# Performance work log

Hardware: AMD Instinct MI355X
Metric: run time of the kernel (lower is better)

## Reference

```python
import jax, jax.numpy as jnp
import numpy as np

N_IN, N_HID, N_OUT = 128, 128, 128
BATCH = 131072

def _linear_params(key, fan_in, fan_out):
    # torch nn.Linear default init: U(-1/sqrt(fan_in), 1/sqrt(fan_in))
    kw, kb = jax.random.split(key)
    bound = 1.0 / np.sqrt(fan_in)
    W = jax.random.uniform(kw, (fan_out, fan_in), jnp.float32, -bound, bound)
    b = jax.random.uniform(kb, (fan_out,), jnp.float32, -bound, bound)
    return W, b

def setup_inputs() -> dict:
    key = jax.random.key(0)
    ks = jax.random.split(key, 6)
    x = jax.random.normal(ks[0], (BATCH, N_IN), jnp.float32)
    hidden = jnp.zeros((BATCH, N_HID), jnp.float32)
    ctx = jnp.zeros((BATCH, N_HID), jnp.float32)
    Wf, bf = _linear_params(ks[1], N_IN + N_HID, N_HID)
    Wi, bi = _linear_params(ks[2], N_IN + N_HID, N_HID)
    Wc, bc = _linear_params(ks[3], N_IN + N_HID, N_HID)
    Wo, bo = _linear_params(ks[4], N_IN + N_HID, N_HID)
    Wfc, bfc = _linear_params(ks[5], N_HID, N_OUT)
    return {"x": x, "hidden": hidden, "ctx": ctx,
            "Wf": Wf, "bf": bf, "Wi": Wi, "bi": bi,
            "Wc": Wc, "bc": bc, "Wo": Wo, "bo": bo,
            "Wfc": Wfc, "bfc": bfc}

def reference(x, hidden, ctx, Wf, bf, Wi, bi, Wc, bc, Wo, bo, Wfc, bfc):
    # cat order matches torch: (hidden, x)
    cat_input = jnp.concatenate([hidden, x], axis=1)  # [B, n_hid+n_in]
    # Stack the four gate weights into one GEMM, then split (same math).
    W4 = jnp.concatenate([Wf, Wi, Wc, Wo], axis=0)    # [4*n_hid, n_hid+n_in]
    b4 = jnp.concatenate([bf, bi, bc, bo], axis=0)
    gates = cat_input @ W4.T + b4                     # [B, 4*n_hid]
    f_lin, i_lin, c_lin, o_lin = jnp.split(gates, 4, axis=1)
    f_t = jax.nn.sigmoid(f_lin)
    i_t = jax.nn.sigmoid(i_lin)
    c_t_temp = jnp.tanh(c_lin)
    ctx_new = f_t * ctx + i_t * c_t_temp
    o_t = jax.nn.sigmoid(o_lin)
    hidden_new = o_t * jnp.tanh(ctx_new)
    out = hidden_new @ Wfc.T + bfc                    # [B, n_out]
    return (out, hidden_new, ctx_new)
```

## Files before the change

### kernel.cpp

```cpp
#include <hip/hip_runtime.h>

#define BATCH   131072
#define NHID    128
#define KDIM    256
#define BM      32
#define TPB     512
#define NBLK    256
#define NTILE   (BATCH / BM)
#define TPBLK   (NTILE / NBLK)

typedef __bf16 bf16_t;
typedef __bf16 bf16x4 __attribute__((ext_vector_type(4)));
typedef __bf16 bf16x8 __attribute__((ext_vector_type(8)));
typedef float  f32x4  __attribute__((ext_vector_type(4)));

__device__ __forceinline__ float fsigmoid(float v) {
    return __builtin_amdgcn_rcpf(1.0f + __builtin_amdgcn_exp2f(v * -1.44269504f));
}
__device__ __forceinline__ float ftanh(float v) {
    return __builtin_fmaf(-2.0f,
        __builtin_amdgcn_rcpf(1.0f + __builtin_amdgcn_exp2f(v * 2.88539008f)), 1.0f);
}
__device__ __forceinline__ f32x4 vsig(f32x4 v) {
    f32x4 r;
    #pragma unroll
    for (int i = 0; i < 4; ++i) r[i] = fsigmoid(v[i]);
    return r;
}
__device__ __forceinline__ f32x4 vtanh(f32x4 v) {
    f32x4 r;
    #pragma unroll
    for (int i = 0; i < 4; ++i) r[i] = ftanh(v[i]);
    return r;
}

__global__ void prep_kernel(const float* __restrict__ Wf, const float* __restrict__ Wi,
                            const float* __restrict__ Wc, const float* __restrict__ Wo,
                            const float* __restrict__ bfp, const float* __restrict__ bip,
                            const float* __restrict__ bcp, const float* __restrict__ bop,
                            const float* __restrict__ Wfc,
                            bf16_t* __restrict__ W4p, float* __restrict__ b4p,
                            bf16_t* __restrict__ Wfcb)
{
    int id = blockIdx.x * 256 + threadIdx.x;
    if (id < 512 * 256) {
        int p = id >> 8, k = id & 255;
        int w = p >> 6, t = (p >> 4) & 3, c = p & 15;
        int j = w * 16 + c;
        const float* W = (t == 0) ? Wf : (t == 1) ? Wi : (t == 2) ? Wc : Wo;
        W4p[id] = (bf16_t)W[j * 256 + k];
        if (k == 0) {
            const float* bs = (t == 0) ? bfp : (t == 1) ? bip : (t == 2) ? bcp : bop;
            b4p[p] = bs[j];
        }
    } else {
        int id2 = id - 512 * 256;
        if (id2 < 128 * 128) Wfcb[id2] = (bf16_t)Wfc[id2];
    }
}

__global__ __launch_bounds__(TPB, 2) void lstm_fused(
    const float* __restrict__ x, const float* __restrict__ hidden, const float* __restrict__ ctx,
    const bf16_t* __restrict__ W4p, const float* __restrict__ b4p,
    const bf16_t* __restrict__ Wfcb, const float* __restrict__ bfc,
    float* __restrict__ out, float* __restrict__ hid_out, float* __restrict__ ctx_out)
{
    __shared__ __align__(16) char lds[2 * 16384 + 2 * 8192];

    const int tid  = threadIdx.x;
    const int lane = tid & 63;
    const int wv   = tid >> 6;
    const int l16  = lane & 15;
    const int lq   = lane >> 4;
    const int tile0 = blockIdx.x * TPBLK;
    const int colb  = wv * 16 + lq * 4;
    const int swzA  = (l16 & 7) << 4;

    const int r_s = tid >> 4;
    const int c_s = tid & 15;
    const int swzS = (r_s & 7) << 4;

    bf16x8 B1[32];
    {
        const bf16_t* Bp = W4p + (wv * 64 + l16) * 256 + lq * 8;
        #pragma unroll
        for (int pm = 0; pm < 4; ++pm)
            #pragma unroll
            for (int ks = 0; ks < 8; ++ks)
                B1[pm * 8 + ks] = *(const bf16x8*)(Bp + pm * 16 * 256 + ks * 32);
    }
    bf16x8 b2r[4];
    {
        const bf16_t* B2 = Wfcb + (wv * 16 + l16) * 128 + lq * 8;
        #pragma unroll
        for (int ks = 0; ks < 4; ++ks) b2r[ks] = *(const bf16x8*)(B2 + ks * 32);
    }
    const f32x4 bf4 = *(const f32x4*)(b4p + wv * 64 +  0 + lq * 4);
    const f32x4 bi4 = *(const f32x4*)(b4p + wv * 64 + 16 + lq * 4);
    const f32x4 bc4 = *(const f32x4*)(b4p + wv * 64 + 32 + lq * 4);
    const f32x4 bo4 = *(const f32x4*)(b4p + wv * 64 + 48 + lq * 4);
    const f32x4 bfc4 = *(const f32x4*)(bfc + colb);

    f32x4 sv0, sv1, sv2, sv3;
    f32x4 ctxA[2], ctxB[2];

    {
        const int grow = tile0 * BM + r_s;
        const float* hrow = hidden + (size_t)grow * NHID + c_s * 4;
        const float* xrow = x      + (size_t)grow * NHID + c_s * 4;
        f32x4 t0 = *(const f32x4*)(hrow);
        f32x4 t1 = *(const f32x4*)(hrow + 64);
        f32x4 t2 = *(const f32x4*)(xrow);
        f32x4 t3 = *(const f32x4*)(xrow + 64);
        char* A0 = lds;
        bf16x4 p0, p1, p2, p3;
        p0[0]=(bf16_t)t0.x; p0[1]=(bf16_t)t0.y; p0[2]=(bf16_t)t0.z; p0[3]=(bf16_t)t0.w;
        p1[0]=(bf16_t)t1.x; p1[1]=(bf16_t)t1.y; p1[2]=(bf16_t)t1.z; p1[3]=(bf16_t)t1.w;
        p2[0]=(bf16_t)t2.x; p2[1]=(bf16_t)t2.y; p2[2]=(bf16_t)t2.z; p2[3]=(bf16_t)t2.w;
        p3[0]=(bf16_t)t3.x; p3[1]=(bf16_t)t3.y; p3[2]=(bf16_t)t3.z; p3[3]=(bf16_t)t3.w;
        *(bf16x4*)(A0 + r_s * 512 + ((c_s * 8 +   0) ^ swzS)) = p0;
        *(bf16x4*)(A0 + r_s * 512 + ((c_s * 8 + 128) ^ swzS)) = p1;
        *(bf16x4*)(A0 + r_s * 512 + ((c_s * 8 + 256) ^ swzS)) = p2;
        *(bf16x4*)(A0 + r_s * 512 + ((c_s * 8 + 384) ^ swzS)) = p3;
    }
    {
        const float* cp = ctx + (size_t)(tile0 * BM) * NHID + colb;
        ctxA[0] = *(const f32x4*)(cp + (size_t)l16 * NHID);
        ctxA[1] = *(const f32x4*)(cp + (size_t)(16 + l16) * NHID);
    }
    __syncthreads();

    for (int t = 0; t < TPBLK; ++t) {
        const int P = t & 1;
        const int row0 = (tile0 + t) * BM;
        char* Asb = lds + P * 16384;
        char* Hsb = lds + 32768 + P * 8192;

        {
            const int tn = (t + 1 < TPBLK) ? t + 1 : TPBLK - 1;
            const int grow = (tile0 + tn) * BM + r_s;
            const float* hrow = hidden + (size_t)grow * NHID + c_s * 4;
            const float* xrow = x      + (size_t)grow * NHID + c_s * 4;
            sv0 = *(const f32x4*)(hrow);
            sv1 = *(const f32x4*)(hrow + 64);
            sv2 = *(const f32x4*)(xrow);
            sv3 = *(const f32x4*)(xrow + 64);
            const float* cp = ctx + (size_t)((tile0 + tn) * BM) * NHID + colb;
            ctxB[0] = *(const f32x4*)(cp + (size_t)l16 * NHID);
            ctxB[1] = *(const f32x4*)(cp + (size_t)(16 + l16) * NHID);
        }

        f32x4 acc[4][2];
        #pragma unroll
        for (int pm = 0; pm < 4; ++pm) {
            acc[pm][0] = f32x4{0.f, 0.f, 0.f, 0.f};
            acc[pm][1] = f32x4{0.f, 0.f, 0.f, 0.f};
        }
        #pragma unroll
        for (int ks = 0; ks < 8; ++ks) {
            const int kb = ks * 64 + lq * 16;
            bf16x8 a0 = *(const bf16x8*)(Asb + l16 * 512        + (kb ^ swzA));
            bf16x8 a1 = *(const bf16x8*)(Asb + (16 + l16) * 512 + (kb ^ swzA));
            #pragma unroll
            for (int pm = 0; pm < 4; ++pm) {
                acc[pm][0] = __builtin_amdgcn_mfma_f32_16x16x32_bf16(B1[pm * 8 + ks], a0, acc[pm][0], 0, 0, 0);
                acc[pm][1] = __builtin_amdgcn_mfma_f32_16x16x32_bf16(B1[pm * 8 + ks], a1, acc[pm][1], 0, 0, 0);
            }
        }

        #pragma unroll
        for (int bn = 0; bn < 2; ++bn) {
            const size_t grow = (size_t)(row0 + bn * 16 + l16) * NHID + colb;
            const f32x4 fv = vsig(acc[0][bn] + bf4);
            const f32x4 iv = vsig(acc[1][bn] + bi4);
            const f32x4 cv = vtanh(acc[2][bn] + bc4);
            const f32x4 ov = vsig(acc[3][bn] + bo4);
            const f32x4 cn = fv * ctxA[bn] + iv * cv;
            const f32x4 hn = ov * vtanh(cn);
            *(f32x4*)(ctx_out + grow) = cn;
            *(f32x4*)(hid_out + grow) = hn;
            bf16x4 hb;
            hb[0] = (bf16_t)hn.x; hb[1] = (bf16_t)hn.y;
            hb[2] = (bf16_t)hn.z; hb[3] = (bf16_t)hn.w;
            const int rh = bn * 16 + l16;
            *(bf16x4*)(Hsb + rh * 256 + ((wv * 32 + lq * 8) ^ ((rh & 7) << 4))) = hb;
        }
        ctxA[0] = ctxB[0];
        ctxA[1] = ctxB[1];

        {
            char* An = lds + (1 - P) * 16384;
            bf16x4 p0, p1, p2, p3;
            p0[0]=(bf16_t)sv0.x; p0[1]=(bf16_t)sv0.y; p0[2]=(bf16_t)sv0.z; p0[3]=(bf16_t)sv0.w;
            p1[0]=(bf16_t)sv1.x; p1[1]=(bf16_t)sv1.y; p1[2]=(bf16_t)sv1.z; p1[3]=(bf16_t)sv1.w;
            p2[0]=(bf16_t)sv2.x; p2[1]=(bf16_t)sv2.y; p2[2]=(bf16_t)sv2.z; p2[3]=(bf16_t)sv2.w;
            p3[0]=(bf16_t)sv3.x; p3[1]=(bf16_t)sv3.y; p3[2]=(bf16_t)sv3.z; p3[3]=(bf16_t)sv3.w;
            *(bf16x4*)(An + r_s * 512 + ((c_s * 8 +   0) ^ swzS)) = p0;
            *(bf16x4*)(An + r_s * 512 + ((c_s * 8 + 128) ^ swzS)) = p1;
            *(bf16x4*)(An + r_s * 512 + ((c_s * 8 + 256) ^ swzS)) = p2;
            *(bf16x4*)(An + r_s * 512 + ((c_s * 8 + 384) ^ swzS)) = p3;
        }

        __syncthreads();

        f32x4 acc2[2];
        acc2[0] = f32x4{0.f, 0.f, 0.f, 0.f};
        acc2[1] = f32x4{0.f, 0.f, 0.f, 0.f};
        #pragma unroll
        for (int ks = 0; ks < 4; ++ks) {
            const int kb = ks * 64 + lq * 16;
            bf16x8 h0 = *(const bf16x8*)(Hsb + l16 * 256        + (kb ^ swzA));
            bf16x8 h1 = *(const bf16x8*)(Hsb + (16 + l16) * 256 + (kb ^ swzA));
            acc2[0] = __builtin_amdgcn_mfma_f32_16x16x32_bf16(b2r[ks], h0, acc2[0], 0, 0, 0);
            acc2[1] = __builtin_amdgcn_mfma_f32_16x16x32_bf16(b2r[ks], h1, acc2[1], 0, 0, 0);
        }
        #pragma unroll
        for (int bn = 0; bn < 2; ++bn) {
            const size_t grow = (size_t)(row0 + bn * 16 + l16) * NHID + colb;
            *(f32x4*)(out + grow) = acc2[bn] + bfc4;
        }
    }
}

extern "C" void kernel_launch(void* const* d_in, const int* in_sizes, int n_in,
                              void* d_out, int out_size, void* d_ws, size_t ws_size,
                              hipStream_t stream) {
    const float* x      = (const float*)d_in[0];
    const float* hidden = (const float*)d_in[1];
    const float* ctx    = (const float*)d_in[2];
    const float* Wf     = (const float*)d_in[3];
    const float* bfp    = (const float*)d_in[4];
    const float* Wi     = (const float*)d_in[5];
    const float* bip    = (const float*)d_in[6];
    const float* Wc     = (const float*)d_in[7];
    const float* bcp    = (const float*)d_in[8];
    const float* Wo     = (const float*)d_in[9];
    const float* bop    = (const float*)d_in[10];
    const float* Wfc    = (const float*)d_in[11];
    const float* bfc    = (const float*)d_in[12];

    bf16_t* W4p  = (bf16_t*)d_ws;
    float*  b4p  = (float*)((char*)d_ws + 512 * 256 * 2);
    bf16_t* Wfcb = (bf16_t*)((char*)d_ws + 512 * 256 * 2 + 2048);

    prep_kernel<<<576, 256, 0, stream>>>(Wf, Wi, Wc, Wo, bfp, bip, bcp, bop, Wfc,
                                         W4p, b4p, Wfcb);

    float* outp = (float*)d_out;
    lstm_fused<<<NBLK, TPB, 0, stream>>>(
        x, hidden, ctx, W4p, b4p, Wfcb, bfc,
        outp,
        outp + (size_t)BATCH * NHID,
        outp + 2 * (size_t)BATCH * NHID);
}
```

Baseline: 117.0 us.

## Stage fp32 input tiles directly into LDS via global_load_lds

Replaces the register-staged load, bf16 convert and LDS store of the hidden/x tile with asynchronous global_load_lds transfers of raw fp32 data into a swizzled LDS buffer. The bf16 conversion moves into the MFMA operand read path. The ctx/hidden output stores are also moved after the barrier. The aim is to free VGPRs and VALU work from staging and overlap loads better, at the cost of doubling LDS footprint (dynamic shared memory) and LDS read traffic, plus extra conversions inside the inner GEMM loop.

```diff
diff --git a/kernel.cpp b/kernel.cpp
--- a/kernel.cpp
+++ b/kernel.cpp
@@ -9,10 +9,17 @@
 #define NTILE   (BATCH / BM)
 #define TPBLK   (NTILE / NBLK)
 
+#define AS_BYTES  (BM * KDIM * 4)
+#define HS_BYTES  (BM * NHID * 2)
+#define LDS_TOTAL (2 * AS_BYTES + 2 * HS_BYTES)
+
 typedef __bf16 bf16_t;
 typedef __bf16 bf16x4 __attribute__((ext_vector_type(4)));
 typedef __bf16 bf16x8 __attribute__((ext_vector_type(8)));
 typedef float  f32x4  __attribute__((ext_vector_type(4)));
+
+#define LDS_AS3(p)  ((__attribute__((address_space(3))) void*)(p))
+#define GLB_AS1(p)  ((const __attribute__((address_space(1))) void*)(p))
 
 __device__ __forceinline__ float fsigmoid(float v) {
     return __builtin_amdgcn_rcpf(1.0f + __builtin_amdgcn_exp2f(v * -1.44269504f));
@@ -65,7 +72,7 @@
     const bf16_t* __restrict__ Wfcb, const float* __restrict__ bfc,
     float* __restrict__ out, float* __restrict__ hid_out, float* __restrict__ ctx_out)
 {
-    __shared__ __align__(16) char lds[2 * 16384 + 2 * 8192];
+    extern __shared__ __align__(16) char smem[];
 
     const int tid  = threadIdx.x;
     const int lane = tid & 63;
@@ -74,11 +81,6 @@
     const int lq   = lane >> 4;
     const int tile0 = blockIdx.x * TPBLK;
     const int colb  = wv * 16 + lq * 4;
-    const int swzA  = (l16 & 7) << 4;
-
-    const int r_s = tid >> 4;
-    const int c_s = tid & 15;
-    const int swzS = (r_s & 7) << 4;
 
     bf16x8 B1[32];
     {
@@ -95,34 +97,29 @@
         #pragma unroll
         for (int ks = 0; ks < 4; ++ks) b2r[ks] = *(const bf16x8*)(B2 + ks * 32);
     }
-    const f32x4 bf4 = *(const f32x4*)(b4p + wv * 64 +  0 + lq * 4);
-    const f32x4 bi4 = *(const f32x4*)(b4p + wv * 64 + 16 + lq * 4);
-    const f32x4 bc4 = *(const f32x4*)(b4p + wv * 64 + 32 + lq * 4);
-    const f32x4 bo4 = *(const f32x4*)(b4p + wv * 64 + 48 + lq * 4);
+    const f32x4 bf4  = *(const f32x4*)(b4p + wv * 64 +  0 + lq * 4);
+    const f32x4 bi4  = *(const f32x4*)(b4p + wv * 64 + 16 + lq * 4);
+    const f32x4 bc4  = *(const f32x4*)(b4p + wv * 64 + 32 + lq * 4);
+    const f32x4 bo4  = *(const f32x4*)(b4p + wv * 64 + 48 + lq * 4);
     const f32x4 bfc4 = *(const f32x4*)(bfc + colb);
 
-    f32x4 sv0, sv1, sv2, sv3;
     f32x4 ctxA[2], ctxB[2];
 
-    {
-        const int grow = tile0 * BM + r_s;
-        const float* hrow = hidden + (size_t)grow * NHID + c_s * 4;
-        const float* xrow = x      + (size_t)grow * NHID + c_s * 4;
-        f32x4 t0 = *(const f32x4*)(hrow);
-        f32x4 t1 = *(const f32x4*)(hrow + 64);
-        f32x4 t2 = *(const f32x4*)(xrow);
-        f32x4 t3 = *(const f32x4*)(xrow + 64);
-        char* A0 = lds;
-        bf16x4 p0, p1, p2, p3;
-        p0[0]=(bf16_t)t0.x; p0[1]=(bf16_t)t0.y; p0[2]=(bf16_t)t0.z; p0[3]=(bf16_t)t0.w;
-        p1[0]=(bf16_t)t1.x; p1[1]=(bf16_t)t1.y; p1[2]=(bf16_t)t1.z; p1[3]=(bf16_t)t1.w;
-        p2[0]=(bf16_t)t2.x; p2[1]=(bf16_t)t2.y; p2[2]=(bf16_t)t2.z; p2[3]=(bf16_t)t2.w;
-        p3[0]=(bf16_t)t3.x; p3[1]=(bf16_t)t3.y; p3[2]=(bf16_t)t3.z; p3[3]=(bf16_t)t3.w;
-        *(bf16x4*)(A0 + r_s * 512 + ((c_s * 8 +   0) ^ swzS)) = p0;
-        *(bf16x4*)(A0 + r_s * 512 + ((c_s * 8 + 128) ^ swzS)) = p1;
-        *(bf16x4*)(A0 + r_s * 512 + ((c_s * 8 + 256) ^ swzS)) = p2;
-        *(bf16x4*)(A0 + r_s * 512 + ((c_s * 8 + 384) ^ swzS)) = p3;
-    }
+    #define STAGE_TILE(An, tt) do {                                             \
+        const int rowb = (tt) * BM;                                             \
+        _Pragma("unroll")                                                       \
+        for (int i = 0; i < 4; ++i) {                                           \
+            const int r = wv * 4 + i;                                           \
+            const int qs = (lane * 16) ^ ((r & 15) << 4);                       \
+            const char* sp = (qs < 512)                                         \
+                ? ((const char*)hidden + (size_t)(rowb + r) * 512 + qs)         \
+                : ((const char*)x      + (size_t)(rowb + r) * 512 + (qs - 512));\
+            __builtin_amdgcn_global_load_lds(GLB_AS1(sp),                       \
+                LDS_AS3((An) + r * 1024), 16, 0, 0);                            \
+        }                                                                       \
+    } while (0)
+
+    STAGE_TILE(smem, tile0 - tile0 + tile0 * 0 + tile0);
     {
         const float* cp = ctx + (size_t)(tile0 * BM) * NHID + colb;
         ctxA[0] = *(const f32x4*)(cp + (size_t)l16 * NHID);
@@ -133,19 +130,14 @@
     for (int t = 0; t < TPBLK; ++t) {
         const int P = t & 1;
         const int row0 = (tile0 + t) * BM;
-        char* Asb = lds + P * 16384;
-        char* Hsb = lds + 32768 + P * 8192;
+        char* Asb = smem + P * AS_BYTES;
+        char* Hsb = smem + 2 * AS_BYTES + P * HS_BYTES;
 
         {
-            const int tn = (t + 1 < TPBLK) ? t + 1 : TPBLK - 1;
-            const int grow = (tile0 + tn) * BM + r_s;
-            const float* hrow = hidden + (size_t)grow * NHID + c_s * 4;
-            const float* xrow = x      + (size_t)grow * NHID + c_s * 4;
-            sv0 = *(const f32x4*)(hrow);
-            sv1 = *(const f32x4*)(hrow + 64);
-            sv2 = *(const f32x4*)(xrow);
-            sv3 = *(const f32x4*)(xrow + 64);
-            const float* cp = ctx + (size_t)((tile0 + tn) * BM) * NHID + colb;
+            const int tn = (t + 1 < TPBLK) ? (tile0 + t + 1) : (tile0 + TPBLK - 1);
+            char* An = smem + (1 - P) * AS_BYTES;
+            STAGE_TILE(An, tn);
+            const float* cp = ctx + (size_t)(tn * BM) * NHID + colb;
             ctxB[0] = *(const f32x4*)(cp + (size_t)l16 * NHID);
             ctxB[1] = *(const f32x4*)(cp + (size_t)(16 + l16) * NHID);
         }
@@ -158,50 +150,53 @@
         }
         #pragma unroll
         for (int ks = 0; ks < 8; ++ks) {
-            const int kb = ks * 64 + lq * 16;
-            bf16x8 a0 = *(const bf16x8*)(Asb + l16 * 512        + (kb ^ swzA));
-            bf16x8 a1 = *(const bf16x8*)(Asb + (16 + l16) * 512 + (kb ^ swzA));
+            const int kb = ks * 128 + lq * 32;
+            bf16x8 a[2];
+            #pragma unroll
+            for (int bn = 0; bn < 2; ++bn) {
+                const int rr = bn * 16 + l16;
+                const char* base = Asb + rr * 1024;
+                const int swz = (rr & 15) << 4;
+                f32x4 f0 = *(const f32x4*)(base + (kb ^ swz));
+                f32x4 f1 = *(const f32x4*)(base + ((kb + 16) ^ swz));
+                a[bn][0] = (bf16_t)f0.x; a[bn][1] = (bf16_t)f0.y;
+                a[bn][2] = (bf16_t)f0.z; a[bn][3] = (bf16_t)f0.w;
+                a[bn][4] = (bf16_t)f1.x; a[bn][5] = (bf16_t)f1.y;
+                a[bn][6] = (bf16_t)f1.z; a[bn][7] = (bf16_t)f1.w;
+            }
             #pragma unroll
             for (int pm = 0; pm < 4; ++pm) {
-                acc[pm][0] = __builtin_amdgcn_mfma_f32_16x16x32_bf16(B1[pm * 8 + ks], a0, acc[pm][0], 0, 0, 0);
-                acc[pm][1] = __builtin_amdgcn_mfma_f32_16x16x32_bf16(B1[pm * 8 + ks], a1, acc[pm][1], 0, 0, 0);
-            }
-        }
-
+                acc[pm][0] = __builtin_amdgcn_mfma_f32_16x16x32_bf16(B1[pm * 8 + ks], a[0], acc[pm][0], 0, 0, 0);
+                acc[pm][1] = __builtin_amdgcn_mfma_f32_16x16x32_bf16(B1[pm * 8 + ks], a[1], acc[pm][1], 0, 0, 0);
+            }
+        }
+
+        f32x4 cn[2], hn[2];
         #pragma unroll
         for (int bn = 0; bn < 2; ++bn) {
-            const size_t grow = (size_t)(row0 + bn * 16 + l16) * NHID + colb;
             const f32x4 fv = vsig(acc[0][bn] + bf4);
             const f32x4 iv = vsig(acc[1][bn] + bi4);
             const f32x4 cv = vtanh(acc[2][bn] + bc4);
             const f32x4 ov = vsig(acc[3][bn] + bo4);
-            const f32x4 cn = fv * ctxA[bn] + iv * cv;
-            const f32x4 hn = ov * vtanh(cn);
-            *(f32x4*)(ctx_out + grow) = cn;
-            *(f32x4*)(hid_out + grow) = hn;
+            cn[bn] = fv * ctxA[bn] + iv * cv;
+            hn[bn] = ov * vtanh(cn[bn]);
             bf16x4 hb;
-            hb[0] = (bf16_t)hn.x; hb[1] = (bf16_t)hn.y;
-            hb[2] = (bf16_t)hn.z; hb[3] = (bf16_t)hn.w;
+            hb[0] = (bf16_t)hn[bn].x; hb[1] = (bf16_t)hn[bn].y;
+            hb[2] = (bf16_t)hn[bn].z; hb[3] = (bf16_t)hn[bn].w;
             const int rh = bn * 16 + l16;
-            *(bf16x4*)(Hsb + rh * 256 + ((wv * 32 + lq * 8) ^ ((rh & 7) << 4))) = hb;
+            *(bf16x4*)(Hsb + rh * 256 + ((wv * 32 + lq * 8) ^ ((rh & 15) << 4))) = hb;
         }
         ctxA[0] = ctxB[0];
         ctxA[1] = ctxB[1];
 
-        {
-            char* An = lds + (1 - P) * 16384;
-            bf16x4 p0, p1, p2, p3;
-            p0[0]=(bf16_t)sv0.x; p0[1]=(bf16_t)sv0.y; p0[2]=(bf16_t)sv0.z; p0[3]=(bf16_t)sv0.w;
-            p1[0]=(bf16_t)sv1.x; p1[1]=(bf16_t)sv1.y; p1[2]=(bf16_t)sv1.z; p1[3]=(bf16_t)sv1.w;
-            p2[0]=(bf16_t)sv2.x; p2[1]=(bf16_t)sv2.y; p2[2]=(bf16_t)sv2.z; p2[3]=(bf16_t)sv2.w;
-            p3[0]=(bf16_t)sv3.x; p3[1]=(bf16_t)sv3.y; p3[2]=(bf16_t)sv3.z; p3[3]=(bf16_t)sv3.w;
-            *(bf16x4*)(An + r_s * 512 + ((c_s * 8 +   0) ^ swzS)) = p0;
-            *(bf16x4*)(An + r_s * 512 + ((c_s * 8 + 128) ^ swzS)) = p1;
-            *(bf16x4*)(An + r_s * 512 + ((c_s * 8 + 256) ^ swzS)) = p2;
-            *(bf16x4*)(An + r_s * 512 + ((c_s * 8 + 384) ^ swzS)) = p3;
-        }
-
         __syncthreads();
+
+        #pragma unroll
+        for (int bn = 0; bn < 2; ++bn) {
+            const size_t grow = (size_t)(row0 + bn * 16 + l16) * NHID + colb;
+            *(f32x4*)(ctx_out + grow) = cn[bn];
+            *(f32x4*)(hid_out + grow) = hn[bn];
+        }
 
         f32x4 acc2[2];
         acc2[0] = f32x4{0.f, 0.f, 0.f, 0.f};
@@ -209,8 +204,15 @@
         #pragma unroll
         for (int ks = 0; ks < 4; ++ks) {
             const int kb = ks * 64 + lq * 16;
-            bf16x8 h0 = *(const bf16x8*)(Hsb + l16 * 256        + (kb ^ swzA));
-            bf16x8 h1 = *(const bf16x8*)(Hsb + (16 + l16) * 256 + (kb ^ swzA));
+            bf16x8 h0, h1;
+            {
+                const int rr = l16;
+                h0 = *(const bf16x8*)(Hsb + rr * 256 + (kb ^ ((rr & 15) << 4)));
+            }
+            {
+                const int rr = 16 + l16;
+                h1 = *(const bf16x8*)(Hsb + rr * 256 + (kb ^ ((rr & 15) << 4)));
+            }
             acc2[0] = __builtin_amdgcn_mfma_f32_16x16x32_bf16(b2r[ks], h0, acc2[0], 0, 0, 0);
             acc2[1] = __builtin_amdgcn_mfma_f32_16x16x32_bf16(b2r[ks], h1, acc2[1], 0, 0, 0);
         }
@@ -220,6 +222,7 @@
             *(f32x4*)(out + grow) = acc2[bn] + bfc4;
         }
     }
+    #undef STAGE_TILE
 }
 
 extern "C" void kernel_launch(void* const* d_in, const int* in_sizes, int n_in,
@@ -243,11 +246,16 @@
     float*  b4p  = (float*)((char*)d_ws + 512 * 256 * 2);
     bf16_t* Wfcb = (bf16_t*)((char*)d_ws + 512 * 256 * 2 + 2048);
 
+    static bool attr_set = false;
+    hipFuncSetAttribute((const void*)lstm_fused,
+                        hipFuncAttributeMaxDynamicSharedMemorySize, LDS_TOTAL);
+    (void)attr_set;
+
     prep_kernel<<<576, 256, 0, stream>>>(Wf, Wi, Wc, Wo, bfp, bip, bcp, bop, Wfc,
                                          W4p, b4p, Wfcb);
 
     float* outp = (float*)d_out;
-    lstm_fused<<<NBLK, TPB, 0, stream>>>(
+    lstm_fused<<<NBLK, TPB, LDS_TOTAL, stream>>>(
         x, hidden, ctx, W4p, b4p, Wfcb, bfc,
         outp,
         outp + (size_t)BATCH * NHID,
```

Result: slower. 202.5 us (+73.0%).
